# Kernel tuning notes

Measured on AMD Instinct MI355X. Metric: run time of the kernel, lower is better.

## Reference

```python
import jax, jax.numpy as jnp
import numpy as np

EPS = 1e-3        # Memory.eps distance threshold
MOMENTUM = 0.999  # Memory.momentum
N, F, M = 500000, 256, 1024


def setup_inputs() -> dict:
    key = jax.random.key(0)
    k1, k2, k3, k4, k5 = jax.random.split(key, 5)
    return {
        "points": jax.random.normal(k1, (M, 3), dtype=jnp.float32),
        "descriptors": jax.random.normal(k2, (M, F), dtype=jnp.float32),
        # learned/stateful memory bank (params/buffers of the module)
        "mem_points": jax.random.normal(k3, (N, 3), dtype=jnp.float32),
        "mem_descriptors": jax.random.normal(k4, (N, F), dtype=jnp.float32),
        "usage": jax.random.randint(k5, (N,), 0, 1000, dtype=jnp.int32),
    }


def _moving(x, m):
    # faithful to Memory.moving: x*m + (1-m)*x  (== x, kept as written)
    return x * m + (1.0 - m) * x


def reference(points, descriptors, mem_points, mem_descriptors, usage):
    # ---- point_address: cdist (p=2) + argmin nearest neighbor ----
    # squared-distance expansion; [M, N] matrix
    d2 = (jnp.sum(points * points, axis=-1)[:, None]
          + jnp.sum(mem_points * mem_points, axis=-1)[None, :]
          - 2.0 * points @ mem_points.T)
    dist = jnp.sqrt(jnp.maximum(d2, 1e-12))
    dmin = jnp.min(dist, axis=-1)
    idx = jnp.argmin(dist, axis=-1)            # [M]
    mask = dmin > EPS                          # queries with no near match

    # ---- topk eviction: lowest-usage slots, assigned in query order ----
    # torch: idx[mask] = usage.topk(k=mask.sum(), largest=False).indices
    # static-shape equivalent: take top-M least-used, select first cumsum(mask)
    _, evict = jax.lax.top_k(-usage, points.shape[0])  # [M] least-used slots
    rank = jnp.cumsum(mask.astype(jnp.int32)) - 1      # position among masked
    idx = jnp.where(mask, evict[rank], idx)

    momentum = jnp.where(mask, 0.0, MOMENTUM)[:, None]  # [M, 1]

    # ---- write: usage bump + momentum scatter-update ----
    usage_new = usage.at[idx].add(1)
    pts_new = mem_points.at[idx].set(_moving(mem_points[idx], momentum))
    desc_new = mem_descriptors.at[idx].set(_moving(mem_descriptors[idx], momentum))

    out = jnp.concatenate([pts_new, desc_new], axis=1)  # [N, 3+F]
    return out, usage_new, idx
```

## Files before the change

### kernel.cpp

```cpp
#include <hip/hip_runtime.h>

#define N_TOT   500000
#define M_Q     1024
#define QB      16
#define NSPLIT  16
#define CAND_MAX 8192

#define COPY_BLKS   2048
#define ARGMIN_BLKS 1024
#define HIST_BLKS   32
#define MEGA_BLKS   (COPY_BLKS + ARGMIN_BLKS + HIST_BLKS)
#define HIST_CHUNK  (N_TOT / HIST_BLKS)

static const unsigned OUT_ROWS  = 259u * (unsigned)N_TOT;
static const unsigned OUT_USAGE = OUT_ROWS;
static const unsigned OUT_IDX   = OUT_ROWS + (unsigned)N_TOT;

#define WS_PARTKEY 0
#define WS_PARTIDX 65536
#define WS_HISTP   131072
#define WS_V       262144
#define WS_CNT     262148
#define WS_KEYS    262152

__global__ __launch_bounds__(256) void k_mega(
    const float* __restrict__ pts,  const float* __restrict__ mpts,
    const float* __restrict__ mdesc, const int* __restrict__ usage,
    float* __restrict__ out,
    float* __restrict__ partKey, int* __restrict__ partIdx,
    int* __restrict__ histPart)
{
    __shared__ int smem[1024];
    const int b   = blockIdx.x;
    const int tid = threadIdx.x;

    if (b < COPY_BLKS) {
        const unsigned TOTQ = (OUT_ROWS + (unsigned)N_TOT) / 4u;
        const unsigned stride = COPY_BLKS * 256u;
        for (unsigned g = (unsigned)b * 256u + tid; g < TOTQ; g += stride) {
            unsigned e = g * 4u;
            float4 v;
            if (e < OUT_ROWS) {
                unsigned n = e / 259u;
                unsigned r = e - n * 259u;
                float tmp[4];
#pragma unroll
                for (int j = 0; j < 4; j++) {
                    tmp[j] = (r < 3u) ? mpts[n * 3u + r] : mdesc[n * 256u + (r - 3u)];
                    r++;
                    if (r == 259u) { r = 0u; n++; }
                }
                v = make_float4(tmp[0], tmp[1], tmp[2], tmp[3]);
            } else {
                unsigned n = e - OUT_ROWS;
                int4 u4 = *reinterpret_cast<const int4*>(usage + n);
                v = make_float4((float)u4.x, (float)u4.y, (float)u4.z, (float)u4.w);
            }
            *reinterpret_cast<float4*>(out + e) = v;
        }
    } else if (b < COPY_BLKS + ARGMIN_BLKS) {
        const int rb = b - COPY_BLKS;
        const int qb = rb & 63;
        const int ns = rb >> 6;
        const int qbase = qb * QB;
        const int chunk = N_TOT / NSPLIT;
        const int n0 = ns * chunk;
        const int n1 = n0 + chunk;

        float* qs = (float*)smem;
        float* wk = (float*)smem + 64;
        int*   wi = smem + 192;
        if (tid < QB * 3) qs[tid] = pts[qbase * 3 + tid];
        __syncthreads();

        float qx[QB], qy[QB], qz[QB];
#pragma unroll
        for (int i = 0; i < QB; i++) { qx[i] = qs[3*i]; qy[i] = qs[3*i+1]; qz[i] = qs[3*i+2]; }

        float bk[QB]; int bi[QB];
#pragma unroll
        for (int i = 0; i < QB; i++) { bk[i] = INFINITY; bi[i] = 0x7fffffff; }

        for (int n = n0 + tid; n < n1; n += 256) {
            float x = mpts[3*n+0], y = mpts[3*n+1], z = mpts[3*n+2];
            float h = 0.5f * (x*x + y*y + z*z);
#pragma unroll
            for (int i = 0; i < QB; i++) {
                float key = h - x*qx[i] - y*qy[i] - z*qz[i];
                bool lt = key < bk[i];
                bk[i] = lt ? key : bk[i];
                bi[i] = lt ? n   : bi[i];
            }
        }

        const int lane = tid & 63;
        const int wv   = tid >> 6;
#pragma unroll
        for (int off = 32; off > 0; off >>= 1) {
#pragma unroll
            for (int i = 0; i < QB; i++) {
                float ok = __shfl_down(bk[i], off, 64);
                int   oi = __shfl_down(bi[i], off, 64);
                if (ok < bk[i] || (ok == bk[i] && oi < bi[i])) { bk[i] = ok; bi[i] = oi; }
            }
        }
        if (lane == 0) {
#pragma unroll
            for (int i = 0; i < QB; i++) { wk[wv*QB + i] = bk[i]; wi[wv*QB + i] = bi[i]; }
        }
        __syncthreads();
        if (tid < QB) {
            float k = wk[tid]; int ix = wi[tid];
#pragma unroll
            for (int w = 1; w < 4; w++) {
                float ok = wk[w*QB + tid]; int oi = wi[w*QB + tid];
                if (ok < k || (ok == k && oi < ix)) { k = ok; ix = oi; }
            }
            partKey[(qbase + tid) * NSPLIT + ns] = k;
            partIdx[(qbase + tid) * NSPLIT + ns] = ix;
        }
    } else {
        const int hb = b - COPY_BLKS - ARGMIN_BLKS;
        const int r0 = hb * HIST_CHUNK;
        const int r1 = r0 + HIST_CHUNK;
#pragma unroll
        for (int i = 0; i < 4; i++) smem[tid + i * 256] = 0;
        __syncthreads();
        for (int n = r0 + tid; n < r1; n += 256) {
            unsigned v = (unsigned)usage[n];
            if (v > 1023u) v = 1023u;
            atomicAdd(&smem[v], 1);
        }
        __syncthreads();
#pragma unroll
        for (int i = 0; i < 4; i++) {
            int bin = tid + i * 256;
            histPart[hb * 1024 + bin] = smem[bin];
        }
    }
}

__global__ __launch_bounds__(1024) void k_scanV(
    const int* __restrict__ histPart, int* __restrict__ Vout, int* __restrict__ cnt)
{
    __shared__ int scan[1024];
    const int t = threadIdx.x;
    int h = 0;
#pragma unroll
    for (int b = 0; b < HIST_BLKS; b++) h += histPart[b * 1024 + t];
    scan[t] = h; __syncthreads();
    for (int off = 1; off < 1024; off <<= 1) {
        int add = (t >= off) ? scan[t - off] : 0;
        __syncthreads();
        scan[t] += add;
        __syncthreads();
    }
    int cum  = scan[t] - h;
    int cumN = scan[t];
    if (cum < M_Q && cumN >= M_Q) { *Vout = t; *cnt = 0; }
}

__global__ __launch_bounds__(256) void k_collect(
    const int* __restrict__ usage, const int* __restrict__ Vp,
    int* __restrict__ cnt, unsigned* __restrict__ keys)
{
    const int V = *Vp;
    const int stride = gridDim.x * 256;
    for (int n = blockIdx.x * 256 + threadIdx.x; n < N_TOT; n += stride) {
        int u = usage[n];
        if (u <= V) {
            int p = atomicAdd(cnt, 1);
            if (p < CAND_MAX) keys[p] = ((unsigned)u << 19) | (unsigned)n;
        }
    }
}

__global__ __launch_bounds__(1024) void k_final(
    const float* __restrict__ pts,
    const float* __restrict__ partKey, const int* __restrict__ partIdx,
    const int* __restrict__ cntP, const unsigned* __restrict__ keysG,
    float* __restrict__ out)
{
    __shared__ unsigned keys[CAND_MAX];
    __shared__ int      mscan[1024];
    const int t = threadIdx.x;

    float bk = INFINITY; int bi = 0x7fffffff;
#pragma unroll
    for (int s = 0; s < NSPLIT; s++) {
        float k = partKey[t * NSPLIT + s];
        int   i = partIdx[t * NSPLIT + s];
        if (k < bk) { bk = k; bi = i; }
    }
    float px = pts[3*t], py = pts[3*t+1], pz = pts[3*t+2];
    float d2 = px*px + py*py + pz*pz + 2.0f * bk;
    const bool mask = d2 > 1e-6f;

    int C = *cntP; if (C > CAND_MAX) C = CAND_MAX;
    int P2 = 1; while (P2 < C) P2 <<= 1;
    for (int p = t; p < P2; p += 1024) keys[p] = (p < C) ? keysG[p] : 0xFFFFFFFFu;
    __syncthreads();

    for (int k = 2; k <= P2; k <<= 1) {
        for (int j = k >> 1; j > 0; j >>= 1) {
            for (int i = t; i < P2; i += 1024) {
                int ixj = i ^ j;
                if (ixj > i) {
                    unsigned a = keys[i], b = keys[ixj];
                    bool up = ((i & k) == 0);
                    if ((a > b) == up) { keys[i] = b; keys[ixj] = a; }
                }
            }
            __syncthreads();
        }
    }

    mscan[t] = mask ? 1 : 0; __syncthreads();
    for (int off = 1; off < 1024; off <<= 1) {
        int add = (t >= off) ? mscan[t - off] : 0;
        __syncthreads();
        mscan[t] += add;
        __syncthreads();
    }
    int rank = mscan[t] - 1;
    int idx = mask ? (int)(keys[rank] & 0x7FFFFu) : bi;
    out[(size_t)OUT_IDX + (size_t)t] = (float)idx;
    atomicAdd(out + OUT_USAGE + idx, 1.0f);
}

extern "C" void kernel_launch(void* const* d_in, const int* in_sizes, int n_in,
                              void* d_out, int out_size, void* d_ws, size_t ws_size,
                              hipStream_t stream)
{
    (void)in_sizes; (void)n_in; (void)out_size; (void)ws_size;
    const float* pts   = (const float*)d_in[0];
    const float* mpts  = (const float*)d_in[2];
    const float* mdesc = (const float*)d_in[3];
    const int*   usage = (const int*)d_in[4];
    float* out = (float*)d_out;

    char* ws = (char*)d_ws;
    float*    partKey  = (float*)(ws + WS_PARTKEY);
    int*      partIdx  = (int*)(ws + WS_PARTIDX);
    int*      histPart = (int*)(ws + WS_HISTP);
    int*      Vp       = (int*)(ws + WS_V);
    int*      cnt      = (int*)(ws + WS_CNT);
    unsigned* keys     = (unsigned*)(ws + WS_KEYS);

    k_mega<<<MEGA_BLKS, 256, 0, stream>>>(pts, mpts, mdesc, usage, out,
                                          partKey, partIdx, histPart);
    k_scanV<<<1, 1024, 0, stream>>>(histPart, Vp, cnt);
    k_collect<<<64, 256, 0, stream>>>(usage, Vp, cnt, keys);
    k_final<<<1, 1024, 0, stream>>>(pts, partKey, partIdx, cnt, keys, out);
}
```

Measured before the change: 347.0 us.

## Stage row-block copy through LDS with vectorized loads and reorder mega-kernel blocks

Replaces the grid-stride scalar-gather copy of the concatenated [N,259] output with per-block tiles of 16 rows. Each tile is loaded as float4 from the descriptors into shared memory, padded with the 3 point coordinates, then written out as contiguous float4s. The usage-to-float conversion moves to its own dedicated blocks. Argmin and histogram blocks are placed first so the long-latency compute starts early. This removes the per-element division and the uncoalesced scalar loads, at the cost of about 31k small blocks, extra LDS traffic and a larger shared allocation that may reduce occupancy for the argmin blocks.

```diff
diff --git a/kernel.cpp b/kernel.cpp
--- a/kernel.cpp
+++ b/kernel.cpp
@@ -6,10 +6,12 @@
 #define NSPLIT  16
 #define CAND_MAX 8192
 
-#define COPY_BLKS   2048
 #define ARGMIN_BLKS 1024
 #define HIST_BLKS   32
-#define MEGA_BLKS   (COPY_BLKS + ARGMIN_BLKS + HIST_BLKS)
+#define USAGE_BLKS  64
+#define CROWS       16
+#define COPY_BLKS   (N_TOT / CROWS)
+#define MEGA_BLKS   (ARGMIN_BLKS + HIST_BLKS + USAGE_BLKS + COPY_BLKS)
 #define HIST_CHUNK  (N_TOT / HIST_BLKS)
 
 static const unsigned OUT_ROWS  = 259u * (unsigned)N_TOT;
@@ -30,46 +32,21 @@
     float* __restrict__ partKey, int* __restrict__ partIdx,
     int* __restrict__ histPart)
 {
-    __shared__ int smem[1024];
+    __shared__ float smem[CROWS * 259];
     const int b   = blockIdx.x;
     const int tid = threadIdx.x;
 
-    if (b < COPY_BLKS) {
-        const unsigned TOTQ = (OUT_ROWS + (unsigned)N_TOT) / 4u;
-        const unsigned stride = COPY_BLKS * 256u;
-        for (unsigned g = (unsigned)b * 256u + tid; g < TOTQ; g += stride) {
-            unsigned e = g * 4u;
-            float4 v;
-            if (e < OUT_ROWS) {
-                unsigned n = e / 259u;
-                unsigned r = e - n * 259u;
-                float tmp[4];
-#pragma unroll
-                for (int j = 0; j < 4; j++) {
-                    tmp[j] = (r < 3u) ? mpts[n * 3u + r] : mdesc[n * 256u + (r - 3u)];
-                    r++;
-                    if (r == 259u) { r = 0u; n++; }
-                }
-                v = make_float4(tmp[0], tmp[1], tmp[2], tmp[3]);
-            } else {
-                unsigned n = e - OUT_ROWS;
-                int4 u4 = *reinterpret_cast<const int4*>(usage + n);
-                v = make_float4((float)u4.x, (float)u4.y, (float)u4.z, (float)u4.w);
-            }
-            *reinterpret_cast<float4*>(out + e) = v;
-        }
-    } else if (b < COPY_BLKS + ARGMIN_BLKS) {
-        const int rb = b - COPY_BLKS;
-        const int qb = rb & 63;
-        const int ns = rb >> 6;
+    if (b < ARGMIN_BLKS) {
+        const int qb = b & 63;
+        const int ns = b >> 6;
         const int qbase = qb * QB;
         const int chunk = N_TOT / NSPLIT;
         const int n0 = ns * chunk;
         const int n1 = n0 + chunk;
 
-        float* qs = (float*)smem;
-        float* wk = (float*)smem + 64;
-        int*   wi = smem + 192;
+        float* qs = smem;
+        float* wk = smem + 64;
+        int*   wi = (int*)(smem + 192);
         if (tid < QB * 3) qs[tid] = pts[qbase * 3 + tid];
         __syncthreads();
 
@@ -119,23 +96,59 @@
             partKey[(qbase + tid) * NSPLIT + ns] = k;
             partIdx[(qbase + tid) * NSPLIT + ns] = ix;
         }
-    } else {
-        const int hb = b - COPY_BLKS - ARGMIN_BLKS;
+    } else if (b < ARGMIN_BLKS + HIST_BLKS) {
+        const int hb = b - ARGMIN_BLKS;
         const int r0 = hb * HIST_CHUNK;
         const int r1 = r0 + HIST_CHUNK;
-#pragma unroll
-        for (int i = 0; i < 4; i++) smem[tid + i * 256] = 0;
+        int* lh = (int*)smem;
+#pragma unroll
+        for (int i = 0; i < 4; i++) lh[tid + i * 256] = 0;
         __syncthreads();
         for (int n = r0 + tid; n < r1; n += 256) {
             unsigned v = (unsigned)usage[n];
             if (v > 1023u) v = 1023u;
-            atomicAdd(&smem[v], 1);
+            atomicAdd(&lh[v], 1);
         }
         __syncthreads();
 #pragma unroll
         for (int i = 0; i < 4; i++) {
             int bin = tid + i * 256;
-            histPart[hb * 1024 + bin] = smem[bin];
+            histPart[hb * 1024 + bin] = lh[bin];
+        }
+    } else if (b < ARGMIN_BLKS + HIST_BLKS + USAGE_BLKS) {
+        const int ub = b - ARGMIN_BLKS - HIST_BLKS;
+        const int4* u4 = (const int4*)usage;
+        float4* o4 = (float4*)(out + OUT_USAGE);
+        const int TOT4 = N_TOT / 4;
+        for (int g = ub * 256 + tid; g < TOT4; g += USAGE_BLKS * 256) {
+            int4 u = u4[g];
+            o4[g] = make_float4((float)u.x, (float)u.y, (float)u.z, (float)u.w);
+        }
+    } else {
+        const int cb = b - (ARGMIN_BLKS + HIST_BLKS + USAGE_BLKS);
+        const int n0 = cb * CROWS;
+        const float4* src = (const float4*)(mdesc + (size_t)n0 * 256);
+#pragma unroll
+        for (int it = 0; it < 4; it++) {
+            int g = tid + it * 256;
+            float4 v = src[g];
+            int e = g * 4;
+            int r = e >> 8;
+            int c = e & 255;
+            float* d = smem + r * 259 + 3 + c;
+            d[0] = v.x; d[1] = v.y; d[2] = v.z; d[3] = v.w;
+        }
+        if (tid < CROWS * 3) {
+            int r = tid / 3, c = tid - r * 3;
+            smem[r * 259 + c] = mpts[(size_t)n0 * 3 + tid];
+        }
+        __syncthreads();
+        float4* dst4 = (float4*)(out + (size_t)cb * (CROWS * 259));
+        const float4* s4 = (const float4*)smem;
+#pragma unroll
+        for (int it = 0; it < 5; it++) {
+            int g = tid + it * 256;
+            if (g < CROWS * 259 / 4) dst4[g] = s4[g];
         }
     }
 }
@@ -206,9 +219,9 @@
             for (int i = t; i < P2; i += 1024) {
                 int ixj = i ^ j;
                 if (ixj > i) {
-                    unsigned a = keys[i], b = keys[ixj];
+                    unsigned a = keys[i], bb = keys[ixj];
                     bool up = ((i & k) == 0);
-                    if ((a > b) == up) { keys[i] = b; keys[ixj] = a; }
+                    if ((a > bb) == up) { keys[i] = bb; keys[ixj] = a; }
                 }
             }
             __syncthreads();
```

Result: faster. 331.7 us (-4.4%).
